# Kernel tuning notes

Measured on AMD Instinct MI355X. Metric: run time of the kernel, lower is better.

The kernel has to match this reference:

```python
import jax, jax.numpy as jnp
import numpy as np


def setup_inputs() -> dict:
    key = jax.random.key(0)
    ks = jax.random.split(key, 5)
    T, B, C, H, K = 2048, 8, 1024, 16, 7
    s = 1.0 / np.sqrt(C)
    return {
        "x": jax.random.normal(ks[0], (T, B, C), dtype=jnp.float32),
        "w_weight": jax.random.normal(ks[1], (H * K, C), dtype=jnp.float32) * s,
        "glu_w": jax.random.normal(ks[2], (2 * H, C), dtype=jnp.float32) * s,
        "glu_b": jnp.zeros((2 * H,), dtype=jnp.float32),
        "out_w": jax.random.normal(ks[3], (C, C), dtype=jnp.float32) * s,
        "out_b": jnp.zeros((C,), dtype=jnp.float32),
        "padding_l": 6,
    }


def reference(x, w_weight, glu_w, glu_b, out_w, out_b, padding_l):
    # x: (T, B, C) in TBC format
    T, B, C = x.shape
    H = glu_w.shape[0] // 2
    K = w_weight.shape[0] // H
    R = C // H  # channels per head

    # GLU gate: C -> 2H, split last dim, a * sigmoid(b)  -> (T, B, H)
    g = (x @ glu_w.T + glu_b).reshape(T, B, H, 2)
    gate = g[..., 0] * jax.nn.sigmoid(g[..., 1])

    # per-position per-head kernel weights, softmax over K -> (T, B, H, K)
    w = jax.nn.softmax((x @ w_weight.T).reshape(T, B, H, K), axis=-1)

    # depthwise dynamic conv: out[t] = sum_k w[t,k] * x_pad[t + k]
    xh = x.reshape(T, B, H, R)
    xp = jnp.pad(xh, ((padding_l, K - 1 - padding_l), (0, 0), (0, 0), (0, 0)))
    conv = jnp.zeros_like(xh)
    for k in range(K):  # K is small & static; avoids (B,H,T,K,R) unfold blowup
        conv = conv + w[..., k:k + 1] * jax.lax.dynamic_slice_in_dim(xp, k, T, axis=0)

    # gate per head, merge heads, output projection
    out = (conv * gate[..., None]).reshape(T, B, C)
    return out @ out_w.T + out_b
```

## Files before the change

### kernel.cpp

```cpp
#include <hip/hip_runtime.h>
#include <hip/hip_bf16.h>
#include <stdint.h>

#define T_DIM 2048
#define B_DIM 8
#define C_DIM 1024
#define H_DIM 16
#define K_DIM 7
#define M_DIM (T_DIM * B_DIM)
#define NLOG 144
#define CW_STRIDE 128

typedef __attribute__((ext_vector_type(8))) short short8;
typedef __attribute__((ext_vector_type(4))) float floatx4;

__device__ __forceinline__ ushort f2bf(float f) {
    __hip_bfloat16 h = __float2bfloat16(f);
    return *(ushort*)&h;
}

#define S_W  ((size_t)112 * C_DIM)
#define S_G  ((size_t)32 * C_DIM)
#define S_O  ((size_t)C_DIM * C_DIM)
#define S_WG (S_W + S_G)
#define S_CVT (S_WG + S_O)

__global__ __launch_bounds__(256) void cvt_w_kernel(
    const float* __restrict__ w_weight, const float* __restrict__ glu_w,
    const float* __restrict__ out_w,
    ushort* __restrict__ wb, ushort* __restrict__ Wb)
{
    size_t gid = ((size_t)blockIdx.x * 256 + threadIdx.x) * 4;
    const float* src; ushort* dst; size_t off;
    if (gid < S_W)            { src = w_weight; dst = wb;       off = gid; }
    else if (gid < S_WG)      { src = glu_w;    dst = wb + S_W; off = gid - S_W; }
    else                      { src = out_w;    dst = Wb;       off = gid - S_WG; }
    float4 v = *(const float4*)(src + off);
    ushort4 o; o.x = f2bf(v.x); o.y = f2bf(v.y); o.z = f2bf(v.z); o.w = f2bf(v.w);
    *(ushort4*)(dst + off) = o;
}

__global__ __launch_bounds__(256) void logits_kernel(
    const float* __restrict__ x,
    const ushort* __restrict__ wb,
    const float* __restrict__ glu_b,
    float* __restrict__ cw)
{
    __shared__ __align__(16) ushort Bs[2][144 * 32];
    __shared__ float lsm[64][NLOG];

    const int tid = threadIdx.x;
    const int wave = tid >> 6, lane = tid & 63;
    const int fr = lane & 15, q = lane >> 4;
    const int m0 = blockIdx.x * 64;
    const int mrow = m0 + wave * 16 + fr;

    floatx4 acc[9];
#pragma unroll
    for (int j = 0; j < 9; ++j) acc[j] = (floatx4){0.f, 0.f, 0.f, 0.f};

    const float* arow = x + (size_t)mrow * C_DIM + q * 8;

    for (int i = tid; i < 576; i += 256) {
        int r = i >> 2, ch = i & 3;
        __builtin_amdgcn_global_load_lds(
            (const __attribute__((address_space(1))) void*)(wb + (size_t)r * C_DIM + ch * 8),
            (__attribute__((address_space(3))) void*)(&Bs[0][0] + i * 8), 16, 0, 0);
    }
    float4 a0 = *(const float4*)(arow);
    float4 a1 = *(const float4*)(arow + 4);
    __syncthreads();

    for (int kc = 0; kc < 32; ++kc) {
        const int buf = kc & 1;
        if (kc < 31) {
            const ushort* wsrc = wb + (kc + 1) * 32;
            for (int i = tid; i < 576; i += 256) {
                int r = i >> 2, ch = i & 3;
                __builtin_amdgcn_global_load_lds(
                    (const __attribute__((address_space(1))) void*)(wsrc + (size_t)r * C_DIM + ch * 8),
                    (__attribute__((address_space(3))) void*)(&Bs[buf ^ 1][0] + i * 8), 16, 0, 0);
            }
        }
        short8 a;
        a[0] = (short)f2bf(a0.x); a[1] = (short)f2bf(a0.y);
        a[2] = (short)f2bf(a0.z); a[3] = (short)f2bf(a0.w);
        a[4] = (short)f2bf(a1.x); a[5] = (short)f2bf(a1.y);
        a[6] = (short)f2bf(a1.z); a[7] = (short)f2bf(a1.w);
        if (kc < 31) {
            a0 = *(const float4*)(arow + (kc + 1) * 32);
            a1 = *(const float4*)(arow + (kc + 1) * 32 + 4);
        }
#pragma unroll
        for (int j = 0; j < 9; ++j) {
            short8 b = *(const short8*)(&Bs[buf][0] + ((j * 16 + fr) * 4 + q) * 8);
            acc[j] = __builtin_amdgcn_mfma_f32_16x16x32_bf16(a, b, acc[j], 0, 0, 0);
        }
        __syncthreads();
    }

#pragma unroll
    for (int j = 0; j < 9; ++j)
#pragma unroll
        for (int r = 0; r < 4; ++r)
            lsm[wave * 16 + q * 4 + r][j * 16 + fr] = acc[j][r];
    __syncthreads();

    {
        const int row = tid >> 2;
        const int hbase = (tid & 3) * 4;
        float* crow = cw + (size_t)(m0 + row) * CW_STRIDE;
#pragma unroll
        for (int hh = 0; hh < 4; ++hh) {
            const int h = hbase + hh;
            float l[K_DIM];
            float mx = -1e30f;
#pragma unroll
            for (int k = 0; k < K_DIM; ++k) { l[k] = lsm[row][h * K_DIM + k]; mx = fmaxf(mx, l[k]); }
            float s = 0.f;
#pragma unroll
            for (int k = 0; k < K_DIM; ++k) { l[k] = __expf(l[k] - mx); s += l[k]; }
            float inv = 1.f / s;
#pragma unroll
            for (int k = 0; k < K_DIM; ++k) crow[h * K_DIM + k] = l[k] * inv;
            float ga = lsm[row][112 + 2 * h] + glu_b[2 * h];
            float gb = lsm[row][113 + 2 * h] + glu_b[2 * h + 1];
            crow[112 + h] = ga * (1.f / (1.f + __expf(-gb)));
        }
    }
}

__global__ __launch_bounds__(256) void conv_kernel(
    const float* __restrict__ x,
    const float* __restrict__ cw,
    const int* __restrict__ padding_l_,
    ushort* __restrict__ y)
{
    const int lb = (blockIdx.x & 7) * 512 + (blockIdx.x >> 3);
    const int wave = threadIdx.x >> 6, lane = threadIdx.x & 63;
    const int m = lb * 4 + wave;
    const int t = m >> 3;
    const int pad = *padding_l_;
    const int h = lane >> 2;

    const float* crow = cw + (size_t)m * CW_STRIDE;
    float wt[K_DIM];
#pragma unroll
    for (int k = 0; k < K_DIM; ++k) wt[k] = crow[h * K_DIM + k];
    const float g = crow[112 + h];

    const int c0 = lane * 16;
    float av[16];
#pragma unroll
    for (int i = 0; i < 16; ++i) av[i] = 0.f;

#pragma unroll
    for (int k = 0; k < K_DIM; ++k) {
        int ts = t + k - pad;
        if (ts < 0 || ts >= T_DIM) continue;
        float wv = wt[k];
        const float4* xp = (const float4*)(x + ((size_t)m + 8 * (k - pad)) * C_DIM + c0);
        float4 u0 = xp[0], u1 = xp[1], u2 = xp[2], u3 = xp[3];
        av[0]  += wv * u0.x; av[1]  += wv * u0.y; av[2]  += wv * u0.z; av[3]  += wv * u0.w;
        av[4]  += wv * u1.x; av[5]  += wv * u1.y; av[6]  += wv * u1.z; av[7]  += wv * u1.w;
        av[8]  += wv * u2.x; av[9]  += wv * u2.y; av[10] += wv * u2.z; av[11] += wv * u2.w;
        av[12] += wv * u3.x; av[13] += wv * u3.y; av[14] += wv * u3.z; av[15] += wv * u3.w;
    }

    uint32_t o[8];
#pragma unroll
    for (int i = 0; i < 8; ++i)
        o[i] = (uint32_t)f2bf(av[2 * i] * g) | ((uint32_t)f2bf(av[2 * i + 1] * g) << 16);
    uint4* yr = (uint4*)(y + (size_t)m * C_DIM + c0);
    yr[0] = (uint4){o[0], o[1], o[2], o[3]};
    yr[1] = (uint4){o[4], o[5], o[6], o[7]};
}

__global__ __launch_bounds__(512, 2) void out_gemm(
    const ushort* __restrict__ y,
    const ushort* __restrict__ Wb,
    const float* __restrict__ bias,
    float* __restrict__ out)
{
    __shared__ __align__(16) ushort SM[3][2][256 * 32];

    const int orig = (blockIdx.x & 7) * 32 + (blockIdx.x >> 3);
    const int bm = orig >> 2;
    const int bn = orig & 3;
    const int m0 = bm * 256, n0 = bn * 256;
    const int tid = threadIdx.x;
    const int lane = tid & 63, wave = tid >> 6;
    const int wr = wave >> 2;
    const int wc = wave & 3;
    const int fr = lane & 15, q = lane >> 4;

    floatx4 acc[8][4];
#pragma unroll
    for (int i = 0; i < 8; ++i)
#pragma unroll
        for (int j = 0; j < 4; ++j) acc[i][j] = (floatx4){0.f, 0.f, 0.f, 0.f};

    auto stage = [&](int buf, int k0) {
#pragma unroll
        for (int j = 0; j < 2; ++j) {
            int idx = j * 512 + tid;
            int r = idx >> 2, cl = idx & 3;
            int ch = cl ^ ((r >> 1) & 3);
            __builtin_amdgcn_global_load_lds(
                (const __attribute__((address_space(1))) void*)(y + (size_t)(m0 + r) * C_DIM + k0 + ch * 8),
                (__attribute__((address_space(3))) void*)(&SM[buf][0][0] + idx * 8), 16, 0, 0);
            __builtin_amdgcn_global_load_lds(
                (const __attribute__((address_space(1))) void*)(Wb + (size_t)(n0 + r) * C_DIM + k0 + ch * 8),
                (__attribute__((address_space(3))) void*)(&SM[buf][1][0] + idx * 8), 16, 0, 0);
        }
    };

    stage(0, 0);
    stage(1, 32);

    int cur = 0;
    for (int kt = 0; kt < 32; ++kt) {
        if (kt + 2 < 32) {
            int stg = cur + 2; if (stg >= 3) stg -= 3;
            stage(stg, (kt + 2) * 32);
        }
        if (kt < 30)       asm volatile("s_waitcnt vmcnt(8)" ::: "memory");
        else if (kt == 30) asm volatile("s_waitcnt vmcnt(4)" ::: "memory");
        else               asm volatile("s_waitcnt vmcnt(0)" ::: "memory");
        __builtin_amdgcn_s_barrier();
        asm volatile("" ::: "memory");

        const ushort* Ab = &SM[cur][0][0];
        const ushort* Bb = &SM[cur][1][0];
        short8 a[8], b[4];
#pragma unroll
        for (int mf = 0; mf < 8; ++mf) {
            int r = wr * 128 + mf * 16 + fr;
            a[mf] = *(const short8*)(Ab + r * 32 + ((q ^ ((r >> 1) & 3)) * 8));
        }
#pragma unroll
        for (int nf = 0; nf < 4; ++nf) {
            int r = wc * 64 + nf * 16 + fr;
            b[nf] = *(const short8*)(Bb + r * 32 + ((q ^ ((r >> 1) & 3)) * 8));
        }
        __builtin_amdgcn_s_setprio(1);
#pragma unroll
        for (int mf = 0; mf < 8; ++mf)
#pragma unroll
            for (int nf = 0; nf < 4; ++nf)
                acc[mf][nf] = __builtin_amdgcn_mfma_f32_16x16x32_bf16(a[mf], b[nf], acc[mf][nf], 0, 0, 0);
        __builtin_amdgcn_s_setprio(0);

        asm volatile("" ::: "memory");
        __builtin_amdgcn_s_barrier();
        asm volatile("" ::: "memory");
        cur = (cur == 2) ? 0 : cur + 1;
    }

#pragma unroll
    for (int nf = 0; nf < 4; ++nf) {
        int n = n0 + wc * 64 + nf * 16 + fr;
        float bv = bias[n];
#pragma unroll
        for (int mf = 0; mf < 8; ++mf) {
#pragma unroll
            for (int r = 0; r < 4; ++r) {
                int m = m0 + wr * 128 + mf * 16 + q * 4 + r;
                out[(size_t)m * C_DIM + n] = acc[mf][nf][r] + bv;
            }
        }
    }
}

extern "C" void kernel_launch(void* const* d_in, const int* in_sizes, int n_in,
                              void* d_out, int out_size, void* d_ws, size_t ws_size,
                              hipStream_t stream) {
    const float* x        = (const float*)d_in[0];
    const float* w_weight = (const float*)d_in[1];
    const float* glu_w    = (const float*)d_in[2];
    const float* glu_b    = (const float*)d_in[3];
    const float* out_w    = (const float*)d_in[4];
    const float* out_b    = (const float*)d_in[5];
    const int* padding_l  = (const int*)d_in[6];
    float* out = (float*)d_out;

    char* ws = (char*)d_ws;
    ushort* y  = (ushort*)ws;
    ushort* wb = y + (size_t)M_DIM * C_DIM;
    ushort* Wb = wb + S_WG;
    float* cwp = (float*)(Wb + S_O);

    cvt_w_kernel<<<S_CVT / 4 / 256, 256, 0, stream>>>(w_weight, glu_w, out_w, wb, Wb);
    logits_kernel<<<M_DIM / 64, 256, 0, stream>>>(x, wb, glu_b, cwp);
    conv_kernel<<<M_DIM / 4, 256, 0, stream>>>(x, cwp, padding_l, y);
    out_gemm<<<(M_DIM / 256) * (C_DIM / 256), 512, 0, stream>>>(y, Wb, out_b, out);
}
```

Measured before the change: 221.5 us.

## Restructure output GEMM into 4-phase ping-pong schedule with BK=64 half-tile staging

```diff
diff --git a/kernel.cpp b/kernel.cpp
--- a/kernel.cpp
+++ b/kernel.cpp
@@ -182,7 +182,7 @@
     const float* __restrict__ bias,
     float* __restrict__ out)
 {
-    __shared__ __align__(16) ushort SM[3][2][256 * 32];
+    __shared__ __align__(16) ushort SM[2][4][128 * 64];
 
     const int orig = (blockIdx.x & 7) * 32 + (blockIdx.x >> 3);
     const int bm = orig >> 2;
@@ -193,6 +193,8 @@
     const int wr = wave >> 2;
     const int wc = wave & 3;
     const int fr = lane & 15, q = lane >> 4;
+    const int g0 = ((q) ^ (fr & 7)) * 8;
+    const int g1 = ((4 + q) ^ (fr & 7)) * 8;
 
     floatx4 acc[8][4];
 #pragma unroll
@@ -200,61 +202,124 @@
 #pragma unroll
         for (int j = 0; j < 4; ++j) acc[i][j] = (floatx4){0.f, 0.f, 0.f, 0.f};
 
-    auto stage = [&](int buf, int k0) {
+    auto stageH = [&](int buf, int mat, int half, int k0) {
+        const ushort* src = mat ? Wb : y;
+        const int row0 = (mat ? n0 : m0) + half * 128;
+        ushort* dst = &SM[buf][mat * 2 + half][0];
 #pragma unroll
         for (int j = 0; j < 2; ++j) {
             int idx = j * 512 + tid;
-            int r = idx >> 2, cl = idx & 3;
-            int ch = cl ^ ((r >> 1) & 3);
+            int r = idx >> 3, gl = idx & 7;
+            int gs = gl ^ (r & 7);
             __builtin_amdgcn_global_load_lds(
-                (const __attribute__((address_space(1))) void*)(y + (size_t)(m0 + r) * C_DIM + k0 + ch * 8),
-                (__attribute__((address_space(3))) void*)(&SM[buf][0][0] + idx * 8), 16, 0, 0);
-            __builtin_amdgcn_global_load_lds(
-                (const __attribute__((address_space(1))) void*)(Wb + (size_t)(n0 + r) * C_DIM + k0 + ch * 8),
-                (__attribute__((address_space(3))) void*)(&SM[buf][1][0] + idx * 8), 16, 0, 0);
+                (const __attribute__((address_space(1))) void*)(src + (size_t)(row0 + r) * C_DIM + k0 + gs * 8),
+                (__attribute__((address_space(3))) void*)(dst + idx * 8), 16, 0, 0);
         }
     };
 
-    stage(0, 0);
-    stage(1, 32);
-
-    int cur = 0;
-    for (int kt = 0; kt < 32; ++kt) {
-        if (kt + 2 < 32) {
-            int stg = cur + 2; if (stg >= 3) stg -= 3;
-            stage(stg, (kt + 2) * 32);
-        }
-        if (kt < 30)       asm volatile("s_waitcnt vmcnt(8)" ::: "memory");
-        else if (kt == 30) asm volatile("s_waitcnt vmcnt(4)" ::: "memory");
-        else               asm volatile("s_waitcnt vmcnt(0)" ::: "memory");
-        __builtin_amdgcn_s_barrier();
-        asm volatile("" ::: "memory");
-
-        const ushort* Ab = &SM[cur][0][0];
-        const ushort* Bb = &SM[cur][1][0];
-        short8 a[8], b[4];
-#pragma unroll
-        for (int mf = 0; mf < 8; ++mf) {
-            int r = wr * 128 + mf * 16 + fr;
-            a[mf] = *(const short8*)(Ab + r * 32 + ((q ^ ((r >> 1) & 3)) * 8));
-        }
-#pragma unroll
-        for (int nf = 0; nf < 4; ++nf) {
-            int r = wc * 64 + nf * 16 + fr;
-            b[nf] = *(const short8*)(Bb + r * 32 + ((q ^ ((r >> 1) & 3)) * 8));
-        }
+    stageH(0, 0, 0, 0);  stageH(0, 0, 1, 0);
+    stageH(0, 1, 0, 0);  stageH(0, 1, 1, 0);
+    stageH(1, 1, 0, 64); stageH(1, 1, 1, 64);
+    asm volatile("s_waitcnt vmcnt(4)" ::: "memory");
+    __builtin_amdgcn_s_barrier();
+    asm volatile("" ::: "memory");
+
+    short8 a[4][2], b[4][2];
+    for (int t = 0; t < 16; ++t) {
+        const int buf = t & 1;
+        const ushort* Ar = &SM[buf][wr][0];
+        const ushort* Br = &SM[buf][2 + (wc >> 1)][0];
+        const int brb = (wc & 1) * 64;
+
+#pragma unroll
+        for (int mf = 0; mf < 4; ++mf) {
+            int ro = (mf * 16 + fr) * 64;
+            a[mf][0] = *(const short8*)(Ar + ro + g0);
+            a[mf][1] = *(const short8*)(Ar + ro + g1);
+        }
+#pragma unroll
+        for (int nf = 0; nf < 2; ++nf) {
+            int ro = (brb + nf * 16 + fr) * 64;
+            b[nf][0] = *(const short8*)(Br + ro + g0);
+            b[nf][1] = *(const short8*)(Br + ro + g1);
+        }
+        if (t + 1 < 16) stageH(buf ^ 1, 0, 0, (t + 1) * 64);
+        __builtin_amdgcn_s_barrier();
+        asm volatile("s_waitcnt lgkmcnt(0)" ::: "memory");
         __builtin_amdgcn_s_setprio(1);
 #pragma unroll
-        for (int mf = 0; mf < 8; ++mf)
-#pragma unroll
-            for (int nf = 0; nf < 4; ++nf)
-                acc[mf][nf] = __builtin_amdgcn_mfma_f32_16x16x32_bf16(a[mf], b[nf], acc[mf][nf], 0, 0, 0);
+        for (int ks = 0; ks < 2; ++ks)
+#pragma unroll
+            for (int mf = 0; mf < 4; ++mf)
+#pragma unroll
+                for (int nf = 0; nf < 2; ++nf)
+                    acc[mf][nf] = __builtin_amdgcn_mfma_f32_16x16x32_bf16(a[mf][ks], b[nf][ks], acc[mf][nf], 0, 0, 0);
         __builtin_amdgcn_s_setprio(0);
-
-        asm volatile("" ::: "memory");
-        __builtin_amdgcn_s_barrier();
-        asm volatile("" ::: "memory");
-        cur = (cur == 2) ? 0 : cur + 1;
+        asm volatile("" ::: "memory");
+        __builtin_amdgcn_s_barrier();
+        asm volatile("" ::: "memory");
+
+#pragma unroll
+        for (int nf = 2; nf < 4; ++nf) {
+            int ro = (brb + nf * 16 + fr) * 64;
+            b[nf][0] = *(const short8*)(Br + ro + g0);
+            b[nf][1] = *(const short8*)(Br + ro + g1);
+        }
+        if (t + 1 < 16) stageH(buf ^ 1, 0, 1, (t + 1) * 64);
+        __builtin_amdgcn_s_barrier();
+        asm volatile("s_waitcnt lgkmcnt(0)" ::: "memory");
+        __builtin_amdgcn_s_setprio(1);
+#pragma unroll
+        for (int ks = 0; ks < 2; ++ks)
+#pragma unroll
+            for (int mf = 0; mf < 4; ++mf)
+#pragma unroll
+                for (int nf = 2; nf < 4; ++nf)
+                    acc[mf][nf] = __builtin_amdgcn_mfma_f32_16x16x32_bf16(a[mf][ks], b[nf][ks], acc[mf][nf], 0, 0, 0);
+        __builtin_amdgcn_s_setprio(0);
+        asm volatile("" ::: "memory");
+        __builtin_amdgcn_s_barrier();
+        asm volatile("" ::: "memory");
+
+#pragma unroll
+        for (int mf = 0; mf < 4; ++mf) {
+            int ro = ((mf + 4) * 16 + fr) * 64;
+            a[mf][0] = *(const short8*)(Ar + ro + g0);
+            a[mf][1] = *(const short8*)(Ar + ro + g1);
+        }
+        if (t + 2 < 16) stageH(buf, 1, 0, (t + 2) * 64);
+        __builtin_amdgcn_s_barrier();
+        asm volatile("s_waitcnt lgkmcnt(0)" ::: "memory");
+        __builtin_amdgcn_s_setprio(1);
+#pragma unroll
+        for (int ks = 0; ks < 2; ++ks)
+#pragma unroll
+            for (int mf = 0; mf < 4; ++mf)
+#pragma unroll
+                for (int nf = 0; nf < 2; ++nf)
+                    acc[mf + 4][nf] = __builtin_amdgcn_mfma_f32_16x16x32_bf16(a[mf][ks], b[nf][ks], acc[mf + 4][nf], 0, 0, 0);
+        __builtin_amdgcn_s_setprio(0);
+        asm volatile("" ::: "memory");
+        __builtin_amdgcn_s_barrier();
+        asm volatile("" ::: "memory");
+
+        if (t + 2 < 16) stageH(buf, 1, 1, (t + 2) * 64);
+        if (t < 14)       { asm volatile("s_waitcnt vmcnt(4)" ::: "memory"); }
+        else if (t == 14) { asm volatile("s_waitcnt vmcnt(0)" ::: "memory"); }
+        __builtin_amdgcn_s_barrier();
+        asm volatile("" ::: "memory");
+        __builtin_amdgcn_s_setprio(1);
+#pragma unroll
+        for (int ks = 0; ks < 2; ++ks)
+#pragma unroll
+            for (int mf = 0; mf < 4; ++mf)
+#pragma unroll
+                for (int nf = 2; nf < 4; ++nf)
+                    acc[mf + 4][nf] = __builtin_amdgcn_mfma_f32_16x16x32_bf16(a[mf][ks], b[nf][ks], acc[mf + 4][nf], 0, 0, 0);
+        __builtin_amdgcn_s_setprio(0);
+        asm volatile("" ::: "memory");
+        __builtin_amdgcn_s_barrier();
+        asm volatile("" ::: "memory");
     }
 
 #pragma unroll
```

New measurement: 216.5 us. -2.2%, faster.
